# Kernel tuning notes

Measured on AMD Instinct MI355X. Metric: run time of the kernel, lower is better.

The kernel has to match this reference:

```python
import jax, jax.numpy as jnp
import numpy as np
import math

T, B, I, N, O = 512, 256, 128, 1024, 10
H_STEP = 0.1
ALPHA = 1.0
OMEGA = 1.0
GAMMA = 0.1
OMEGA_FACTOR = OMEGA * OMEGA
GAMMA_FACTOR = 2.0 * GAMMA
GAIN_REC = 1.0 / math.sqrt(N)


def setup_inputs() -> dict:
    key = jax.random.key(0)
    ks = jax.random.split(key, 7)
    # torch.nn.Linear default init: U(-1/sqrt(fan_in), 1/sqrt(fan_in))
    def lin(kw, kb, fan_out, fan_in):
        bound = 1.0 / math.sqrt(fan_in)
        w = jax.random.uniform(kw, (fan_out, fan_in), minval=-bound, maxval=bound, dtype=jnp.float32)
        b = jax.random.uniform(kb, (fan_out,), minval=-bound, maxval=bound, dtype=jnp.float32)
        return w, b
    i2h_w, i2h_b = lin(ks[0], ks[1], N, I)
    h2h_w, h2h_b = lin(ks[2], ks[3], N, N)
    h2o_w, h2o_b = lin(ks[4], ks[5], O, N)
    batch = jax.random.normal(ks[6], (T, B, I), dtype=jnp.float32)
    return {
        "batch": batch,
        "i2h_w": i2h_w, "i2h_b": i2h_b,
        "h2h_w": h2h_w, "h2h_b": h2h_b,
        "h2o_w": h2o_w, "h2o_b": h2o_b,
    }


def reference(batch, i2h_w, i2h_b, h2h_w, h2h_b, h2o_w, h2o_b):
    # Precompute input projection for all timesteps: [T, B, N]
    inp_proj = jnp.einsum('tbi,ni->tbn', batch, i2h_w) + i2h_b

    def step(carry, u_t):
        x_t, y_t = carry  # each [B, N]
        rec = GAIN_REC * (y_t @ h2h_w.T + h2h_b)  # gain scales full h2h(y) incl. bias
        y_t = y_t + H_STEP * (ALPHA * jnp.tanh(u_t + rec)
                              - OMEGA_FACTOR * x_t - GAMMA_FACTOR * y_t)
        x_t = x_t + H_STEP * y_t
        return (x_t, y_t), None

    x0 = jnp.zeros((batch.shape[1], h2h_w.shape[0]), dtype=batch.dtype)
    y0 = jnp.zeros_like(x0)
    (x_T, _), _ = jax.lax.scan(step, (x0, y0), inp_proj)
    output = x_T @ h2o_w.T + h2o_b  # [B, O]
    return output
```

## Files before the change

kernel.cpp:

```cpp
#include <hip/hip_runtime.h>

#define T_STEPS 512
#define BATCH_N 256
#define IDIM    128
#define NDIM    1024
#define ODIM    10

#define THREADS 512
#define GAIN 0.03125f

#define YBUF_OFF    (33554432ull)
#define YBUF_HALF   (524288ull)
#define YHALF_EL    (262144u)
#define FLG_OFF     (YBUF_OFF + 2*YBUF_HALF)
#define FLG_BYTES   (1024ull)
#define XT_OFF      (FLG_OFF + FLG_BYTES)
#define XT_BYTES    (1048576ull)
#define WS_NEED     (XT_OFF + XT_BYTES)

typedef short    s16x8 __attribute__((ext_vector_type(8)));
typedef float    f32x4 __attribute__((ext_vector_type(4)));
typedef unsigned u32x4 __attribute__((ext_vector_type(4)));

__device__ __forceinline__ unsigned short f2bf(float f) {
  unsigned u = __builtin_bit_cast(unsigned, f);
  u += 0x7fffu + ((u >> 16) & 1u);
  return (unsigned short)(u >> 16);
}

__global__ void horn_convert(const float* __restrict__ src, unsigned short* __restrict__ dst) {
  size_t gid = (size_t)blockIdx.x * 256 + threadIdx.x;
  const f32x4* s4 = reinterpret_cast<const f32x4*>(src) + gid * 2;
  f32x4 a = s4[0], b = s4[1];
  u32x4 o;
  o[0] = (unsigned)f2bf(a[0]) | ((unsigned)f2bf(a[1]) << 16);
  o[1] = (unsigned)f2bf(a[2]) | ((unsigned)f2bf(a[3]) << 16);
  o[2] = (unsigned)f2bf(b[0]) | ((unsigned)f2bf(b[1]) << 16);
  o[3] = (unsigned)f2bf(b[2]) | ((unsigned)f2bf(b[3]) << 16);
  reinterpret_cast<u32x4*>(dst)[gid] = o;
}

__launch_bounds__(THREADS, 2)
__global__ void horn_persistent(const unsigned short* __restrict__ batchbf,
                                const float* __restrict__ i2h_w,
                                const float* __restrict__ i2h_b,
                                const float* __restrict__ h2h_w,
                                const float* __restrict__ h2h_b,
                                unsigned short* ybuf,
                                unsigned int*  flags,
                                float* xT)
{
  extern __shared__ char smem[];
  char*  ylds = smem;
  f32x4* red  = (f32x4*)(smem + 32768);

  const int tid  = threadIdx.x;
  const int lane = tid & 63;
  const int wv   = tid >> 6;
  const int ki   = wv & 3;
  const int ci   = wv >> 2;
  const int g    = blockIdx.x & 15;
  const int s    = blockIdx.x >> 4;
  const int l15  = lane & 15;
  const int kb   = lane >> 4;
  const int ct_own = ci * 4 + ki;
  const int jc   = s * 128 + ct_own * 16 + l15;

  s16x8 wfrag[4][8];
  #pragma unroll
  for (int j = 0; j < 4; ++j) {
    #pragma unroll
    for (int kc = 0; kc < 8; ++kc) {
      const float* gp = h2h_w + (size_t)(s * 128 + (ci * 4 + j) * 16 + l15) * NDIM
                        + ki * 256 + kc * 32 + kb * 8;
      f32x4 a = *reinterpret_cast<const f32x4*>(gp);
      f32x4 b = *reinterpret_cast<const f32x4*>(gp + 4);
      s16x8 v;
      v[0] = (short)f2bf(a[0]*GAIN); v[1] = (short)f2bf(a[1]*GAIN);
      v[2] = (short)f2bf(a[2]*GAIN); v[3] = (short)f2bf(a[3]*GAIN);
      v[4] = (short)f2bf(b[0]*GAIN); v[5] = (short)f2bf(b[1]*GAIN);
      v[6] = (short)f2bf(b[2]*GAIN); v[7] = (short)f2bf(b[3]*GAIN);
      wfrag[j][kc] = v;
    }
  }

  s16x8 i2hf[4];
  #pragma unroll
  for (int kc = 0; kc < 4; ++kc) {
    const float* gp = i2h_w + (size_t)jc * IDIM + kc * 32 + kb * 8;
    s16x8 v;
    #pragma unroll
    for (int e = 0; e < 8; ++e) v[e] = (short)f2bf(gp[e]);
    i2hf[kc] = v;
  }
  const float bias = i2h_b[jc] + GAIN * h2h_b[jc];

  s16x8 bfr[4];
  {
    const unsigned short* bp = batchbf + ((size_t)g * 16 + l15) * IDIM + kb * 8;
    #pragma unroll
    for (int kc = 0; kc < 4; ++kc) bfr[kc] = *reinterpret_cast<const s16x8*>(bp + kc * 32);
  }

  float xs[4] = {0.f,0.f,0.f,0.f};
  float ys[4] = {0.f,0.f,0.f,0.f};

  const char* ytile = (const char*)ybuf + (size_t)g * 32768;
  unsigned short* pub0 = ybuf + (size_t)(g * 16 + kb * 4) * 1024 + jc;
  const unsigned* fpoll = flags + g * 16 + (lane & 7);
  unsigned* fstore = flags + g * 16 + s;

  for (int t = 0; t < T_STEPS; ++t) {
    const int p = t & 1, pn = p ^ 1;

    if (t > 0) {
      while (true) {
        unsigned fv;
        asm volatile("global_load_dword %0, %1, off sc0 sc1\n\t"
                     "s_waitcnt vmcnt(0)"
                     : "=v"(fv) : "v"(fpoll) : "memory");
        if (__all((int)fv >= t)) break;
        __builtin_amdgcn_s_sleep(1);
      }
    }

    const char* q0 = ytile + (size_t)p * YBUF_HALF + tid * 16;
    u32x4 v0, v1, v2, v3;
    asm volatile(
      "global_load_dwordx4 %0, %4, off sc0 sc1\n\t"
      "global_load_dwordx4 %1, %5, off sc0 sc1\n\t"
      "global_load_dwordx4 %2, %6, off sc0 sc1\n\t"
      "global_load_dwordx4 %3, %7, off sc0 sc1"
      : "=&v"(v0), "=&v"(v1), "=&v"(v2), "=&v"(v3)
      : "v"(q0), "v"(q0 + 8192), "v"(q0 + 16384), "v"(q0 + 24576)
      : "memory");

    f32x4 uacc = {bias, bias, bias, bias};
    #pragma unroll
    for (int kc = 0; kc < 4; ++kc)
      uacc = __builtin_amdgcn_mfma_f32_16x16x32_bf16(bfr[kc], i2hf[kc], uacc, 0, 0, 0);

    {
      const int tn = (t + 1 < T_STEPS) ? (t + 1) : t;
      const unsigned short* bp = batchbf + ((size_t)tn * BATCH_N + g * 16 + l15) * IDIM + kb * 8;
      #pragma unroll
      for (int kc = 0; kc < 4; ++kc) bfr[kc] = *reinterpret_cast<const s16x8*>(bp + kc * 32);
    }

    asm volatile("s_waitcnt vmcnt(0)" ::: "memory");
    __builtin_amdgcn_sched_barrier(0);

    #define STG(r, vr) { int off = tid * 16 + (r) * 8192; int row = off >> 11; \
      *reinterpret_cast<u32x4*>(ylds + (off ^ ((row & 7) << 4))) = vr; }
    STG(0, v0) STG(1, v1) STG(2, v2) STG(3, v3)
    #undef STG
    __syncthreads();

    f32x4 c0 = {0,0,0,0}, c1 = {0,0,0,0}, c2 = {0,0,0,0}, c3 = {0,0,0,0};
    #pragma unroll
    for (int kc = 0; kc < 8; ++kc) {
      int boff = (l15 * 2048 + ki * 512 + kc * 64 + kb * 16) ^ ((l15 & 7) << 4);
      s16x8 a = *reinterpret_cast<const s16x8*>(ylds + boff);
      c0 = __builtin_amdgcn_mfma_f32_16x16x32_bf16(a, wfrag[0][kc], c0, 0, 0, 0);
      c1 = __builtin_amdgcn_mfma_f32_16x16x32_bf16(a, wfrag[1][kc], c1, 0, 0, 0);
      c2 = __builtin_amdgcn_mfma_f32_16x16x32_bf16(a, wfrag[2][kc], c2, 0, 0, 0);
      c3 = __builtin_amdgcn_mfma_f32_16x16x32_bf16(a, wfrag[3][kc], c3, 0, 0, 0);
    }

    red[((size_t)ki * 8 + ci * 4 + 0) * 64 + lane] = c0;
    red[((size_t)ki * 8 + ci * 4 + 1) * 64 + lane] = c1;
    red[((size_t)ki * 8 + ci * 4 + 2) * 64 + lane] = c2;
    red[((size_t)ki * 8 + ci * 4 + 3) * 64 + lane] = c3;
    __syncthreads();
    f32x4 z = uacc;
    z += red[(0 * 8 + ct_own) * 64 + lane];
    z += red[(1 * 8 + ct_own) * 64 + lane];
    z += red[(2 * 8 + ct_own) * 64 + lane];
    z += red[(3 * 8 + ct_own) * 64 + lane];

    unsigned yw0, yw1, yw2, yw3;
    {
      float zz, e, r, th, yn;
      zz = z[0]; e = __expf(zz + zz); r = __builtin_amdgcn_rcpf(e + 1.0f); th = fmaf(-2.0f, r, 1.0f);
      yn = ys[0] + 0.1f*(th - xs[0] - 0.2f*ys[0]); xs[0] += 0.1f*yn; ys[0] = yn; yw0 = f2bf(yn);
      zz = z[1]; e = __expf(zz + zz); r = __builtin_amdgcn_rcpf(e + 1.0f); th = fmaf(-2.0f, r, 1.0f);
      yn = ys[1] + 0.1f*(th - xs[1] - 0.2f*ys[1]); xs[1] += 0.1f*yn; ys[1] = yn; yw1 = f2bf(yn);
      zz = z[2]; e = __expf(zz + zz); r = __builtin_amdgcn_rcpf(e + 1.0f); th = fmaf(-2.0f, r, 1.0f);
      yn = ys[2] + 0.1f*(th - xs[2] - 0.2f*ys[2]); xs[2] += 0.1f*yn; ys[2] = yn; yw2 = f2bf(yn);
      zz = z[3]; e = __expf(zz + zz); r = __builtin_amdgcn_rcpf(e + 1.0f); th = fmaf(-2.0f, r, 1.0f);
      yn = ys[3] + 0.1f*(th - xs[3] - 0.2f*ys[3]); xs[3] += 0.1f*yn; ys[3] = yn; yw3 = f2bf(yn);
    }

    {
      unsigned short* b0 = pub0 + (size_t)pn * YHALF_EL;
      unsigned short* b1 = b0 + 2 * NDIM;
      asm volatile(
        "global_store_short %4, %0, off offset:0    sc0 sc1\n\t"
        "global_store_short %4, %1, off offset:2048 sc0 sc1\n\t"
        "global_store_short %5, %2, off offset:0    sc0 sc1\n\t"
        "global_store_short %5, %3, off offset:2048 sc0 sc1\n\t"
        "s_waitcnt vmcnt(0)"
        :
        : "v"(yw0), "v"(yw1), "v"(yw2), "v"(yw3), "v"(b0), "v"(b1)
        : "memory");
    }
    __syncthreads();
    if (tid == 0) {
      unsigned nv = (unsigned)(t + 1);
      asm volatile("global_store_dword %0, %1, off sc0 sc1"
                   :: "v"(fstore), "v"(nv) : "memory");
    }
  }

  #pragma unroll
  for (int q = 0; q < 4; ++q) {
    int row = g * 16 + kb * 4 + q;
    xT[(size_t)row * NDIM + jc] = xs[q];
  }
}

__global__ void horn_out(const float* __restrict__ xT, const float* __restrict__ h2o_w,
                         const float* __restrict__ h2o_b, float* __restrict__ out) {
  int b = blockIdx.x;
  int lane = threadIdx.x;
  float p[ODIM];
  #pragma unroll
  for (int o = 0; o < ODIM; ++o) p[o] = 0.f;
  for (int it = 0; it < NDIM / 64; ++it) {
    int n = it * 64 + lane;
    float xv = xT[(size_t)b * NDIM + n];
    #pragma unroll
    for (int o = 0; o < ODIM; ++o) p[o] += xv * h2o_w[o * NDIM + n];
  }
  #pragma unroll
  for (int o = 0; o < ODIM; ++o) {
    float v = p[o];
    #pragma unroll
    for (int off = 32; off >= 1; off >>= 1) v += __shfl_down(v, off, 64);
    if (lane == 0) out[b * ODIM + o] = v + h2o_b[o];
  }
}

__global__ void horn_fail(float* out) {
  int i = blockIdx.x * 256 + threadIdx.x;
  if (i < BATCH_N * ODIM) out[i] = 12345.0f;
}

extern "C" void kernel_launch(void* const* d_in, const int* in_sizes, int n_in,
                              void* d_out, int out_size, void* d_ws, size_t ws_size,
                              hipStream_t stream) {
  const float* batch = (const float*)d_in[0];
  const float* i2h_w = (const float*)d_in[1];
  const float* i2h_b = (const float*)d_in[2];
  const float* h2h_w = (const float*)d_in[3];
  const float* h2h_b = (const float*)d_in[4];
  const float* h2o_w = (const float*)d_in[5];
  const float* h2o_b = (const float*)d_in[6];
  float* out = (float*)d_out;
  char* ws = (char*)d_ws;

  if (ws_size < WS_NEED) {
    horn_fail<<<16, 256, 0, stream>>>(out);
    return;
  }

  (void)hipFuncSetAttribute(reinterpret_cast<const void*>(horn_persistent),
                            hipFuncAttributeMaxDynamicSharedMemorySize, 65536);

  hipMemsetAsync(ws + YBUF_OFF, 0, YBUF_HALF, stream);
  hipMemsetAsync(ws + FLG_OFF, 0, FLG_BYTES, stream);

  horn_convert<<<8192, 256, 0, stream>>>(batch, (unsigned short*)(ws + 0));

  horn_persistent<<<128, THREADS, 65536, stream>>>(
      (const unsigned short*)(ws + 0), i2h_w, i2h_b, h2h_w, h2h_b,
      (unsigned short*)(ws + YBUF_OFF), (unsigned int*)(ws + FLG_OFF),
      (float*)(ws + XT_OFF));

  horn_out<<<BATCH_N, 64, 0, stream>>>((const float*)(ws + XT_OFF), h2o_w, h2o_b, out);
}
```

Measured before the change: 1.877 ms.

## Replace flag-based inter-block sync with per-element tagged y words

Each y value is now published as a 32-bit word that packs the bf16 value with a timestep tag. Consumers poll the data itself and retry until every tag reaches the current step. This removes the separate flag poll, the store drain wait, the block barrier and the flag store before the next step, which shortens the critical path of each recurrent step. In exchange each step moves twice as many bytes, adds unpack work, and loses the batch prefetch overlap.

```diff
diff --git a/kernel.cpp b/kernel.cpp
--- a/kernel.cpp
+++ b/kernel.cpp
@@ -10,23 +10,22 @@
 #define GAIN 0.03125f
 
 #define YBUF_OFF    (33554432ull)
-#define YBUF_HALF   (524288ull)
-#define YHALF_EL    (262144u)
-#define FLG_OFF     (YBUF_OFF + 2*YBUF_HALF)
-#define FLG_BYTES   (1024ull)
-#define XT_OFF      (FLG_OFF + FLG_BYTES)
+#define YPAR_WORDS  (262144u)
+#define XT_OFF      (YBUF_OFF + 2097152ull)
 #define XT_BYTES    (1048576ull)
 #define WS_NEED     (XT_OFF + XT_BYTES)
 
 typedef short    s16x8 __attribute__((ext_vector_type(8)));
 typedef float    f32x4 __attribute__((ext_vector_type(4)));
 typedef unsigned u32x4 __attribute__((ext_vector_type(4)));
+typedef unsigned u32x2 __attribute__((ext_vector_type(2)));
 
 __device__ __forceinline__ unsigned short f2bf(float f) {
   unsigned u = __builtin_bit_cast(unsigned, f);
   u += 0x7fffu + ((u >> 16) & 1u);
   return (unsigned short)(u >> 16);
 }
+__device__ __forceinline__ unsigned umin2(unsigned a, unsigned b) { return a < b ? a : b; }
 
 __global__ void horn_convert(const float* __restrict__ src, unsigned short* __restrict__ dst) {
   size_t gid = (size_t)blockIdx.x * 256 + threadIdx.x;
@@ -46,8 +45,7 @@
                                 const float* __restrict__ i2h_b,
                                 const float* __restrict__ h2h_w,
                                 const float* __restrict__ h2h_b,
-                                unsigned short* ybuf,
-                                unsigned int*  flags,
+                                unsigned* ybuf,
                                 float* xT)
 {
   extern __shared__ char smem[];
@@ -105,54 +103,57 @@
   float xs[4] = {0.f,0.f,0.f,0.f};
   float ys[4] = {0.f,0.f,0.f,0.f};
 
-  const char* ytile = (const char*)ybuf + (size_t)g * 32768;
-  unsigned short* pub0 = ybuf + (size_t)(g * 16 + kb * 4) * 1024 + jc;
-  const unsigned* fpoll = flags + g * 16 + (lane & 7);
-  unsigned* fstore = flags + g * 16 + s;
+  const char* gb = (const char*)ybuf + (size_t)g * 65536 + (size_t)tid * 16;
+  unsigned* pb0 = ybuf + (size_t)(g * 16 + kb * 4) * 1024 + jc;
 
   for (int t = 0; t < T_STEPS; ++t) {
     const int p = t & 1, pn = p ^ 1;
-
-    if (t > 0) {
-      while (true) {
-        unsigned fv;
-        asm volatile("global_load_dword %0, %1, off sc0 sc1\n\t"
-                     "s_waitcnt vmcnt(0)"
-                     : "=v"(fv) : "v"(fpoll) : "memory");
-        if (__all((int)fv >= t)) break;
-        __builtin_amdgcn_s_sleep(1);
-      }
-    }
-
-    const char* q0 = ytile + (size_t)p * YBUF_HALF + tid * 16;
-    u32x4 v0, v1, v2, v3;
-    asm volatile(
-      "global_load_dwordx4 %0, %4, off sc0 sc1\n\t"
-      "global_load_dwordx4 %1, %5, off sc0 sc1\n\t"
-      "global_load_dwordx4 %2, %6, off sc0 sc1\n\t"
-      "global_load_dwordx4 %3, %7, off sc0 sc1"
-      : "=&v"(v0), "=&v"(v1), "=&v"(v2), "=&v"(v3)
-      : "v"(q0), "v"(q0 + 8192), "v"(q0 + 16384), "v"(q0 + 24576)
-      : "memory");
-
+    const char* a0 = gb + (size_t)p * 1048576;
+
+    u32x4 g0, g1, g2, g3, g4, g5, g6, g7;
+    #define GISSUE asm volatile( \
+      "global_load_dwordx4 %0, %8, off sc0 sc1\n\t" \
+      "global_load_dwordx4 %1, %9, off sc0 sc1\n\t" \
+      "global_load_dwordx4 %2, %10, off sc0 sc1\n\t" \
+      "global_load_dwordx4 %3, %11, off sc0 sc1\n\t" \
+      "global_load_dwordx4 %4, %12, off sc0 sc1\n\t" \
+      "global_load_dwordx4 %5, %13, off sc0 sc1\n\t" \
+      "global_load_dwordx4 %6, %14, off sc0 sc1\n\t" \
+      "global_load_dwordx4 %7, %15, off sc0 sc1" \
+      : "=&v"(g0), "=&v"(g1), "=&v"(g2), "=&v"(g3), \
+        "=&v"(g4), "=&v"(g5), "=&v"(g6), "=&v"(g7) \
+      : "v"(a0), "v"(a0 + 8192), "v"(a0 + 16384), "v"(a0 + 24576), \
+        "v"(a0 + 32768), "v"(a0 + 40960), "v"(a0 + 49152), "v"(a0 + 57344) \
+      : "memory")
+
+    GISSUE;
     f32x4 uacc = {bias, bias, bias, bias};
     #pragma unroll
     for (int kc = 0; kc < 4; ++kc)
       uacc = __builtin_amdgcn_mfma_f32_16x16x32_bf16(bfr[kc], i2hf[kc], uacc, 0, 0, 0);
 
-    {
-      const int tn = (t + 1 < T_STEPS) ? (t + 1) : t;
-      const unsigned short* bp = batchbf + ((size_t)tn * BATCH_N + g * 16 + l15) * IDIM + kb * 8;
-      #pragma unroll
-      for (int kc = 0; kc < 4; ++kc) bfr[kc] = *reinterpret_cast<const s16x8*>(bp + kc * 32);
-    }
-
-    asm volatile("s_waitcnt vmcnt(0)" ::: "memory");
-    __builtin_amdgcn_sched_barrier(0);
-
-    #define STG(r, vr) { int off = tid * 16 + (r) * 8192; int row = off >> 11; \
-      *reinterpret_cast<u32x4*>(ylds + (off ^ ((row & 7) << 4))) = vr; }
-    STG(0, v0) STG(1, v1) STG(2, v2) STG(3, v3)
+    while (true) {
+      asm volatile("s_waitcnt vmcnt(0)" ::: "memory");
+      __builtin_amdgcn_sched_barrier(0);
+      unsigned mn = 0xffffffffu;
+      #define MN(v) mn = umin2(mn, umin2(umin2(v[0]&0xffffu, v[1]&0xffffu), umin2(v[2]&0xffffu, v[3]&0xffffu)));
+      MN(g0) MN(g1) MN(g2) MN(g3) MN(g4) MN(g5) MN(g6) MN(g7)
+      #undef MN
+      if (__all((int)(mn >= (unsigned)t))) break;
+      __builtin_amdgcn_s_sleep(2);
+      GISSUE;
+    }
+    #undef GISSUE
+
+    #define STG(r, vr) { \
+      u32x2 w_; \
+      w_[0] = __builtin_amdgcn_perm(vr[1], vr[0], 0x07060302u); \
+      w_[1] = __builtin_amdgcn_perm(vr[3], vr[2], 0x07060302u); \
+      int B_ = (r) * 8192 + tid * 16; \
+      int off_ = (B_ >> 1) ^ ((((B_ >> 12) & 7)) << 4); \
+      *reinterpret_cast<u32x2*>(ylds + off_) = w_; }
+    STG(0, g0) STG(1, g1) STG(2, g2) STG(3, g3)
+    STG(4, g4) STG(5, g5) STG(6, g6) STG(7, g7)
     #undef STG
     __syncthreads();
 
@@ -178,37 +179,25 @@
     z += red[(2 * 8 + ct_own) * 64 + lane];
     z += red[(3 * 8 + ct_own) * 64 + lane];
 
-    unsigned yw0, yw1, yw2, yw3;
+    const unsigned tag = (unsigned)(t + 1);
+    unsigned* pb = pb0 + (size_t)pn * YPAR_WORDS;
+    #define UPD(r) { \
+      float z_ = z[r]; \
+      float e_ = __expf(z_ + z_); \
+      float th_ = fmaf(-2.0f, __builtin_amdgcn_rcpf(e_ + 1.0f), 1.0f); \
+      float yn_ = ys[r] + 0.1f*(th_ - xs[r] - 0.2f*ys[r]); \
+      xs[r] += 0.1f*yn_; ys[r] = yn_; \
+      unsigned w_ = ((unsigned)f2bf(yn_) << 16) | tag; \
+      unsigned* ad_ = pb + (r) * 1024; \
+      asm volatile("global_store_dword %0, %1, off sc0 sc1" :: "v"(ad_), "v"(w_) : "memory"); }
+    UPD(0) UPD(1) UPD(2) UPD(3)
+    #undef UPD
+
     {
-      float zz, e, r, th, yn;
-      zz = z[0]; e = __expf(zz + zz); r = __builtin_amdgcn_rcpf(e + 1.0f); th = fmaf(-2.0f, r, 1.0f);
-      yn = ys[0] + 0.1f*(th - xs[0] - 0.2f*ys[0]); xs[0] += 0.1f*yn; ys[0] = yn; yw0 = f2bf(yn);
-      zz = z[1]; e = __expf(zz + zz); r = __builtin_amdgcn_rcpf(e + 1.0f); th = fmaf(-2.0f, r, 1.0f);
-      yn = ys[1] + 0.1f*(th - xs[1] - 0.2f*ys[1]); xs[1] += 0.1f*yn; ys[1] = yn; yw1 = f2bf(yn);
-      zz = z[2]; e = __expf(zz + zz); r = __builtin_amdgcn_rcpf(e + 1.0f); th = fmaf(-2.0f, r, 1.0f);
-      yn = ys[2] + 0.1f*(th - xs[2] - 0.2f*ys[2]); xs[2] += 0.1f*yn; ys[2] = yn; yw2 = f2bf(yn);
-      zz = z[3]; e = __expf(zz + zz); r = __builtin_amdgcn_rcpf(e + 1.0f); th = fmaf(-2.0f, r, 1.0f);
-      yn = ys[3] + 0.1f*(th - xs[3] - 0.2f*ys[3]); xs[3] += 0.1f*yn; ys[3] = yn; yw3 = f2bf(yn);
-    }
-
-    {
-      unsigned short* b0 = pub0 + (size_t)pn * YHALF_EL;
-      unsigned short* b1 = b0 + 2 * NDIM;
-      asm volatile(
-        "global_store_short %4, %0, off offset:0    sc0 sc1\n\t"
-        "global_store_short %4, %1, off offset:2048 sc0 sc1\n\t"
-        "global_store_short %5, %2, off offset:0    sc0 sc1\n\t"
-        "global_store_short %5, %3, off offset:2048 sc0 sc1\n\t"
-        "s_waitcnt vmcnt(0)"
-        :
-        : "v"(yw0), "v"(yw1), "v"(yw2), "v"(yw3), "v"(b0), "v"(b1)
-        : "memory");
-    }
-    __syncthreads();
-    if (tid == 0) {
-      unsigned nv = (unsigned)(t + 1);
-      asm volatile("global_store_dword %0, %1, off sc0 sc1"
-                   :: "v"(fstore), "v"(nv) : "memory");
+      const int tn = (t + 1 < T_STEPS) ? (t + 1) : t;
+      const unsigned short* bp = batchbf + ((size_t)tn * BATCH_N + g * 16 + l15) * IDIM + kb * 8;
+      #pragma unroll
+      for (int kc = 0; kc < 4; ++kc) bfr[kc] = *reinterpret_cast<const s16x8*>(bp + kc * 32);
     }
   }
 
@@ -267,15 +256,13 @@
   (void)hipFuncSetAttribute(reinterpret_cast<const void*>(horn_persistent),
                             hipFuncAttributeMaxDynamicSharedMemorySize, 65536);
 
-  hipMemsetAsync(ws + YBUF_OFF, 0, YBUF_HALF, stream);
-  hipMemsetAsync(ws + FLG_OFF, 0, FLG_BYTES, stream);
+  hipMemsetAsync(ws + YBUF_OFF, 0, 2097152, stream);
 
   horn_convert<<<8192, 256, 0, stream>>>(batch, (unsigned short*)(ws + 0));
 
   horn_persistent<<<128, THREADS, 65536, stream>>>(
       (const unsigned short*)(ws + 0), i2h_w, i2h_b, h2h_w, h2h_b,
-      (unsigned short*)(ws + YBUF_OFF), (unsigned int*)(ws + FLG_OFF),
-      (float*)(ws + XT_OFF));
+      (unsigned*)(ws + YBUF_OFF), (float*)(ws + XT_OFF));
 
   horn_out<<<BATCH_N, 64, 0, stream>>>((const float*)(ws + XT_OFF), h2o_w, h2o_b, out);
 }
```

New measurement: 2.153 ms. +14.7%, slower.

## Split persistent RNN across 256 smaller blocks with single-wave flag polling

Applied to the files above, without the earlier changes.

Repartitions the persistent recurrent kernel from 128 blocks of 512 threads (128 output columns each) to 256 blocks of 256 threads (64 columns each), so each batch group now waits on 16 producer flags instead of 8. Only wave 0 polls the flags, and the other waves wait at a barrier, which cuts polling traffic. The next-step batch prefetch is moved to run after the y stores so it overlaps with them. The change spreads the per-step work over more CUs, at the cost of more inter-block synchronization and a wider dependency fan-in per step. It also relies on all 256 blocks being co-resident.

```diff
diff --git a/kernel.cpp b/kernel.cpp
--- a/kernel.cpp
+++ b/kernel.cpp
@@ -6,14 +6,14 @@
 #define NDIM    1024
 #define ODIM    10
 
-#define THREADS 512
+#define THREADS 256
 #define GAIN 0.03125f
 
 #define YBUF_OFF    (33554432ull)
 #define YBUF_HALF   (524288ull)
 #define YHALF_EL    (262144u)
 #define FLG_OFF     (YBUF_OFF + 2*YBUF_HALF)
-#define FLG_BYTES   (1024ull)
+#define FLG_BYTES   (2048ull)
 #define XT_OFF      (FLG_OFF + FLG_BYTES)
 #define XT_BYTES    (1048576ull)
 #define WS_NEED     (XT_OFF + XT_BYTES)
@@ -40,7 +40,7 @@
   reinterpret_cast<u32x4*>(dst)[gid] = o;
 }
 
-__launch_bounds__(THREADS, 2)
+__launch_bounds__(THREADS, 1)
 __global__ void horn_persistent(const unsigned short* __restrict__ batchbf,
                                 const float* __restrict__ i2h_w,
                                 const float* __restrict__ i2h_b,
@@ -50,29 +50,26 @@
                                 unsigned int*  flags,
                                 float* xT)
 {
-  extern __shared__ char smem[];
-  char*  ylds = smem;
-  f32x4* red  = (f32x4*)(smem + 32768);
+  __shared__ char  ylds[32768];
+  __shared__ f32x4 red[4][4][64];
 
   const int tid  = threadIdx.x;
   const int lane = tid & 63;
   const int wv   = tid >> 6;
-  const int ki   = wv & 3;
-  const int ci   = wv >> 2;
-  const int g    = blockIdx.x & 15;
-  const int s    = blockIdx.x >> 4;
+  const int blk  = blockIdx.x;
+  const int ig   = blk & 15;
+  const int jg   = blk >> 4;
   const int l15  = lane & 15;
   const int kb   = lane >> 4;
-  const int ct_own = ci * 4 + ki;
-  const int jc   = s * 128 + ct_own * 16 + l15;
+  const int jc   = jg * 64 + wv * 16 + l15;
 
   s16x8 wfrag[4][8];
   #pragma unroll
-  for (int j = 0; j < 4; ++j) {
+  for (int ct = 0; ct < 4; ++ct) {
     #pragma unroll
     for (int kc = 0; kc < 8; ++kc) {
-      const float* gp = h2h_w + (size_t)(s * 128 + (ci * 4 + j) * 16 + l15) * NDIM
-                        + ki * 256 + kc * 32 + kb * 8;
+      const float* gp = h2h_w + (size_t)(jg * 64 + ct * 16 + l15) * NDIM
+                        + wv * 256 + kc * 32 + kb * 8;
       f32x4 a = *reinterpret_cast<const f32x4*>(gp);
       f32x4 b = *reinterpret_cast<const f32x4*>(gp + 4);
       s16x8 v;
@@ -80,7 +77,7 @@
       v[2] = (short)f2bf(a[2]*GAIN); v[3] = (short)f2bf(a[3]*GAIN);
       v[4] = (short)f2bf(b[0]*GAIN); v[5] = (short)f2bf(b[1]*GAIN);
       v[6] = (short)f2bf(b[2]*GAIN); v[7] = (short)f2bf(b[3]*GAIN);
-      wfrag[j][kc] = v;
+      wfrag[ct][kc] = v;
     }
   }
 
@@ -97,7 +94,7 @@
 
   s16x8 bfr[4];
   {
-    const unsigned short* bp = batchbf + ((size_t)g * 16 + l15) * IDIM + kb * 8;
+    const unsigned short* bp = batchbf + ((size_t)ig * 16 + l15) * IDIM + kb * 8;
     #pragma unroll
     for (int kc = 0; kc < 4; ++kc) bfr[kc] = *reinterpret_cast<const s16x8*>(bp + kc * 32);
   }
@@ -105,34 +102,43 @@
   float xs[4] = {0.f,0.f,0.f,0.f};
   float ys[4] = {0.f,0.f,0.f,0.f};
 
-  const char* ytile = (const char*)ybuf + (size_t)g * 32768;
-  unsigned short* pub0 = ybuf + (size_t)(g * 16 + kb * 4) * 1024 + jc;
-  const unsigned* fpoll = flags + g * 16 + (lane & 7);
-  unsigned* fstore = flags + g * 16 + s;
+  const char* ytile = (const char*)ybuf + (size_t)ig * 32768;
+  unsigned short* pub0 = ybuf + (size_t)(ig * 16 + kb * 4) * 1024 + jc;
+  const unsigned* fline = flags + ig * 32 + l15;
+  unsigned* fstore = flags + ig * 32 + jg;
 
   for (int t = 0; t < T_STEPS; ++t) {
     const int p = t & 1, pn = p ^ 1;
 
     if (t > 0) {
-      while (true) {
-        unsigned fv;
-        asm volatile("global_load_dword %0, %1, off sc0 sc1\n\t"
-                     "s_waitcnt vmcnt(0)"
-                     : "=v"(fv) : "v"(fpoll) : "memory");
-        if (__all((int)fv >= t)) break;
-        __builtin_amdgcn_s_sleep(1);
+      if (wv == 0) {
+        while (true) {
+          unsigned fv;
+          asm volatile("global_load_dword %0, %1, off sc0 sc1\n\t"
+                       "s_waitcnt vmcnt(0)"
+                       : "=v"(fv) : "v"(fline) : "memory");
+          if (__all((int)fv >= t)) break;
+          __builtin_amdgcn_s_sleep(1);
+        }
       }
+      __syncthreads();
     }
 
     const char* q0 = ytile + (size_t)p * YBUF_HALF + tid * 16;
-    u32x4 v0, v1, v2, v3;
+    u32x4 v0, v1, v2, v3, v4, v5, v6, v7;
     asm volatile(
-      "global_load_dwordx4 %0, %4, off sc0 sc1\n\t"
-      "global_load_dwordx4 %1, %5, off sc0 sc1\n\t"
-      "global_load_dwordx4 %2, %6, off sc0 sc1\n\t"
-      "global_load_dwordx4 %3, %7, off sc0 sc1"
-      : "=&v"(v0), "=&v"(v1), "=&v"(v2), "=&v"(v3)
-      : "v"(q0), "v"(q0 + 8192), "v"(q0 + 16384), "v"(q0 + 24576)
+      "global_load_dwordx4 %0, %8, off sc0 sc1\n\t"
+      "global_load_dwordx4 %1, %9, off sc0 sc1\n\t"
+      "global_load_dwordx4 %2, %10, off sc0 sc1\n\t"
+      "global_load_dwordx4 %3, %11, off sc0 sc1\n\t"
+      "global_load_dwordx4 %4, %12, off sc0 sc1\n\t"
+      "global_load_dwordx4 %5, %13, off sc0 sc1\n\t"
+      "global_load_dwordx4 %6, %14, off sc0 sc1\n\t"
+      "global_load_dwordx4 %7, %15, off sc0 sc1"
+      : "=&v"(v0), "=&v"(v1), "=&v"(v2), "=&v"(v3),
+        "=&v"(v4), "=&v"(v5), "=&v"(v6), "=&v"(v7)
+      : "v"(q0), "v"(q0 + 4096), "v"(q0 + 8192), "v"(q0 + 12288),
+        "v"(q0 + 16384), "v"(q0 + 20480), "v"(q0 + 24576), "v"(q0 + 28672)
       : "memory");
 
     f32x4 uacc = {bias, bias, bias, bias};
@@ -140,26 +146,20 @@
     for (int kc = 0; kc < 4; ++kc)
       uacc = __builtin_amdgcn_mfma_f32_16x16x32_bf16(bfr[kc], i2hf[kc], uacc, 0, 0, 0);
 
-    {
-      const int tn = (t + 1 < T_STEPS) ? (t + 1) : t;
-      const unsigned short* bp = batchbf + ((size_t)tn * BATCH_N + g * 16 + l15) * IDIM + kb * 8;
-      #pragma unroll
-      for (int kc = 0; kc < 4; ++kc) bfr[kc] = *reinterpret_cast<const s16x8*>(bp + kc * 32);
-    }
-
     asm volatile("s_waitcnt vmcnt(0)" ::: "memory");
     __builtin_amdgcn_sched_barrier(0);
 
-    #define STG(r, vr) { int off = tid * 16 + (r) * 8192; int row = off >> 11; \
-      *reinterpret_cast<u32x4*>(ylds + (off ^ ((row & 7) << 4))) = vr; }
+    #define STG(r, vr) { int B_ = (r) * 4096 + tid * 16; int row_ = B_ >> 11; \
+      *reinterpret_cast<u32x4*>(ylds + (B_ ^ ((row_ & 7) << 4))) = vr; }
     STG(0, v0) STG(1, v1) STG(2, v2) STG(3, v3)
+    STG(4, v4) STG(5, v5) STG(6, v6) STG(7, v7)
     #undef STG
     __syncthreads();
 
     f32x4 c0 = {0,0,0,0}, c1 = {0,0,0,0}, c2 = {0,0,0,0}, c3 = {0,0,0,0};
     #pragma unroll
     for (int kc = 0; kc < 8; ++kc) {
-      int boff = (l15 * 2048 + ki * 512 + kc * 64 + kb * 16) ^ ((l15 & 7) << 4);
+      int boff = (l15 * 2048 + wv * 512 + kc * 64 + kb * 16) ^ ((l15 & 7) << 4);
       s16x8 a = *reinterpret_cast<const s16x8*>(ylds + boff);
       c0 = __builtin_amdgcn_mfma_f32_16x16x32_bf16(a, wfrag[0][kc], c0, 0, 0, 0);
       c1 = __builtin_amdgcn_mfma_f32_16x16x32_bf16(a, wfrag[1][kc], c1, 0, 0, 0);
@@ -167,16 +167,16 @@
       c3 = __builtin_amdgcn_mfma_f32_16x16x32_bf16(a, wfrag[3][kc], c3, 0, 0, 0);
     }
 
-    red[((size_t)ki * 8 + ci * 4 + 0) * 64 + lane] = c0;
-    red[((size_t)ki * 8 + ci * 4 + 1) * 64 + lane] = c1;
-    red[((size_t)ki * 8 + ci * 4 + 2) * 64 + lane] = c2;
-    red[((size_t)ki * 8 + ci * 4 + 3) * 64 + lane] = c3;
+    red[wv][0][lane] = c0;
+    red[wv][1][lane] = c1;
+    red[wv][2][lane] = c2;
+    red[wv][3][lane] = c3;
     __syncthreads();
     f32x4 z = uacc;
-    z += red[(0 * 8 + ct_own) * 64 + lane];
-    z += red[(1 * 8 + ct_own) * 64 + lane];
-    z += red[(2 * 8 + ct_own) * 64 + lane];
-    z += red[(3 * 8 + ct_own) * 64 + lane];
+    z += red[0][wv][lane];
+    z += red[1][wv][lane];
+    z += red[2][wv][lane];
+    z += red[3][wv][lane];
 
     unsigned yw0, yw1, yw2, yw3;
     {
@@ -198,12 +198,18 @@
         "global_store_short %4, %0, off offset:0    sc0 sc1\n\t"
         "global_store_short %4, %1, off offset:2048 sc0 sc1\n\t"
         "global_store_short %5, %2, off offset:0    sc0 sc1\n\t"
-        "global_store_short %5, %3, off offset:2048 sc0 sc1\n\t"
-        "s_waitcnt vmcnt(0)"
+        "global_store_short %5, %3, off offset:2048 sc0 sc1"
         :
         : "v"(yw0), "v"(yw1), "v"(yw2), "v"(yw3), "v"(b0), "v"(b1)
         : "memory");
     }
+    {
+      const int tn = (t + 1 < T_STEPS) ? (t + 1) : t;
+      const unsigned short* bp = batchbf + ((size_t)tn * BATCH_N + ig * 16 + l15) * IDIM + kb * 8;
+      #pragma unroll
+      for (int kc = 0; kc < 4; ++kc) bfr[kc] = *reinterpret_cast<const s16x8*>(bp + kc * 32);
+    }
+    asm volatile("s_waitcnt vmcnt(0)" ::: "memory");
     __syncthreads();
     if (tid == 0) {
       unsigned nv = (unsigned)(t + 1);
@@ -214,7 +220,7 @@
 
   #pragma unroll
   for (int q = 0; q < 4; ++q) {
-    int row = g * 16 + kb * 4 + q;
+    int row = ig * 16 + kb * 4 + q;
     xT[(size_t)row * NDIM + jc] = xs[q];
   }
 }
@@ -264,15 +270,12 @@
     return;
   }
 
-  (void)hipFuncSetAttribute(reinterpret_cast<const void*>(horn_persistent),
-                            hipFuncAttributeMaxDynamicSharedMemorySize, 65536);
-
   hipMemsetAsync(ws + YBUF_OFF, 0, YBUF_HALF, stream);
   hipMemsetAsync(ws + FLG_OFF, 0, FLG_BYTES, stream);
 
   horn_convert<<<8192, 256, 0, stream>>>(batch, (unsigned short*)(ws + 0));
 
-  horn_persistent<<<128, THREADS, 65536, stream>>>(
+  horn_persistent<<<256, THREADS, 0, stream>>>(
       (const unsigned short*)(ws + 0), i2h_w, i2h_b, h2h_w, h2h_b,
       (unsigned short*)(ws + YBUF_OFF), (unsigned int*)(ws + FLG_OFF),
       (float*)(ws + XT_OFF));
```

New measurement: 1.522 ms. 18.9% less time.
